# Performance work log

Hardware: AMD Instinct MI355X
Metric: run time of the kernel (lower is better)

## Reference

```python
import jax, jax.numpy as jnp
import numpy as np

N_NODES = 100000


def _deg_norm(idx, n):
    # inverse-sqrt degree, zero-degree nodes -> 0 (DGL norm='both' convention)
    deg = jax.ops.segment_sum(jnp.ones(idx.shape, jnp.float32), idx, num_segments=n)
    return jnp.where(deg > 0, jax.lax.rsqrt(jnp.maximum(deg, 1.0)), 0.0)


def graph_conv(x, src, dst, W, b, n):
    # symmetric normalization: D_out^{-1/2} on src, D_in^{-1/2} on dst
    norm_src = _deg_norm(src, n)  # [N]
    norm_dst = _deg_norm(dst, n)  # [N]
    h = (x * norm_src[:, None]) @ W          # apply weight first (in >= out)
    msg = h[src]                              # gather [E, out]
    agg = jax.ops.segment_sum(msg, dst, num_segments=n)  # scatter-add [N, out]
    return agg * norm_dst[:, None] + b


def setup_inputs() -> dict:
    key = jax.random.key(0)
    ks = jax.random.split(key, 6)
    x = jax.random.normal(ks[0], (N_NODES, 128), dtype=jnp.float32)
    edge_index = jax.random.randint(ks[1], (2, 1600000), 0, N_NODES, dtype=jnp.int64)
    W1 = jax.random.normal(ks[2], (128, 64), dtype=jnp.float32) * (1.0 / np.sqrt(128))
    b1 = jnp.zeros((64,), jnp.float32)
    W2 = jax.random.normal(ks[3], (64, 32), dtype=jnp.float32) * (1.0 / np.sqrt(64))
    b2 = jnp.zeros((32,), jnp.float32)
    Wl = jax.random.normal(ks[4], (32, 1), dtype=jnp.float32) * (1.0 / np.sqrt(32))
    bl = jnp.zeros((1,), jnp.float32)
    return {"x": x, "edge_index": edge_index, "W1": W1, "b1": b1,
            "W2": W2, "b2": b2, "Wl": Wl, "bl": bl}


def reference(x, edge_index, W1, b1, W2, b2, Wl, bl):
    src, dst = edge_index[0], edge_index[1]
    n = x.shape[0]
    h = graph_conv(x, src, dst, W1, b1, n)
    h = jax.nn.relu(h)
    # dropout(p=0.5) is identity at inference
    h = graph_conv(h, src, dst, W2, b2, n)
    return h @ Wl + bl  # [N, 1]
```

## Files before the change

### kernel.cpp

```cpp
#include <hip/hip_runtime.h>
#include <hip/hip_fp16.h>


#define WAVE 64
#define NRANGE 8
#define NQUAD 2
#define CB 1024

typedef _Float16 f16x8 __attribute__((ext_vector_type(8)));
typedef float f32x4 __attribute__((ext_vector_type(4)));

__global__ __launch_bounds__(256) void k_hist(const int* __restrict__ srcArr,
                                              const int* __restrict__ dstArr,
                                              unsigned* __restrict__ partial_s,
                                              unsigned* __restrict__ partial_d,
                                              int E, int B, int C, int chunkE) {
    extern __shared__ unsigned hist[];
    const int q = blockIdx.x & (NQUAD - 1);
    const int c = blockIdx.x >> 1;
    const int lo = q * 4 * B;
    const int* nodes = blockIdx.y ? dstArr : srcArr;
    unsigned* partial = blockIdx.y ? partial_d : partial_s;

    for (int b = threadIdx.x; b < B; b += 256) hist[b] = 0u;
    __syncthreads();

    const int beg = c * chunkE, end = min(beg + chunkE, E);
    const int n4 = (end - beg) >> 2;
    const int4* p = (const int4*)(nodes + beg);
    for (int j = threadIdx.x; j < n4; j += 256) {
        int4 v = p[j];
#pragma unroll
        for (int k = 0; k < 4; ++k) {
            int a = (&v.x)[k] - lo;
            if ((unsigned)a < (unsigned)(4 * B)) {
                int h2 = (a >= 2 * B);
                int r2 = a - (h2 ? 2 * B : 0);
                int h1 = (r2 >= B);
                int bin = r2 - (h1 ? B : 0);
                atomicAdd(&hist[bin], 1u << (((h2 << 1) | h1) << 3));
            }
        }
    }
    for (int j = beg + (n4 << 2) + threadIdx.x; j < end; j += 256) {
        int a = nodes[j] - lo;
        if ((unsigned)a < (unsigned)(4 * B)) {
            int h2 = (a >= 2 * B);
            int r2 = a - (h2 ? 2 * B : 0);
            int h1 = (r2 >= B);
            int bin = r2 - (h1 ? B : 0);
            atomicAdd(&hist[bin], 1u << (((h2 << 1) | h1) << 3));
        }
    }
    __syncthreads();
    unsigned* outp = partial + (size_t)(q * C + c) * B;
    for (int b = threadIdx.x; b < B; b += 256) outp[b] = hist[b];
}

__global__ __launch_bounds__(256) void k_reduce_norm(const unsigned* __restrict__ partial_s,
                                                     unsigned* __restrict__ partial_d,
                                                     float* __restrict__ norm_s,
                                                     float* __restrict__ norm_d,
                                                     unsigned* __restrict__ deg_d,
                                                     int N, int B, int C) {
    int t = blockIdx.x * 256 + threadIdx.x;
    if (t >= NQUAD * B) return;
    int q = t / B, b = t - q * B;
    size_t base = (size_t)(q * C) * B + b;
    unsigned ds = 0;
    for (int c = 0; c < C; ++c) ds += partial_s[base + (size_t)c * B];
    unsigned run = 0;
    for (int c = 0; c < C; ++c) {
        size_t ix = base + (size_t)c * B;
        unsigned v = partial_d[ix];
        partial_d[ix] = run;
        run += v;
    }
#pragma unroll
    for (int j = 0; j < 4; ++j) {
        int n = q * 4 * B + j * B + b;
        if (n < N) {
            unsigned d0 = (ds >> (8 * j)) & 0xffu;
            unsigned d1 = (run >> (8 * j)) & 0xffu;
            deg_d[n] = d1;
            norm_s[n] = d0 ? rsqrtf((float)d0) : 0.0f;
            norm_d[n] = d1 ? rsqrtf((float)d1) : 0.0f;
        }
    }
}

__global__ __launch_bounds__(256) void k_prep(const float* __restrict__ W1,
                                              const float* __restrict__ W2,
                                              const float* __restrict__ b2,
                                              const float* __restrict__ Wl,
                                              const float* __restrict__ bl,
                                              _Float16* __restrict__ wt,
                                              float* __restrict__ w2l,
                                              float* __restrict__ c0) {
    int t = threadIdx.x;
    for (int i = 0; i < 32; ++i) {
        int e = i * 256 + t;
        int k = e >> 6, n = e & 63;
        wt[n * 128 + k] = (_Float16)W1[e];
    }
    if (t < 64) {
        float acc = 0.f;
#pragma unroll
        for (int j = 0; j < 32; ++j) acc += W2[t * 32 + j] * Wl[j];
        w2l[t] = acc;
    }
    if (t == 0) {
        float s = 0.f;
#pragma unroll
        for (int j = 0; j < 32; ++j) s += b2[j] * Wl[j];
        *c0 = s + bl[0];
    }
}

__global__ __launch_bounds__(256) void k_blocksum(const unsigned* __restrict__ deg,
                                                  unsigned* __restrict__ partial, int N) {
    __shared__ unsigned sw[4];
    int i = blockIdx.x * 256 + threadIdx.x;
    unsigned v = (i < N) ? deg[i] : 0u;
#pragma unroll
    for (int off = 32; off; off >>= 1) v += __shfl_xor((int)v, off);
    if ((threadIdx.x & 63) == 0) sw[threadIdx.x >> 6] = v;
    __syncthreads();
    if (threadIdx.x == 0) partial[blockIdx.x] = sw[0] + sw[1] + sw[2] + sw[3];
}

__global__ __launch_bounds__(512) void k_scanpartial(const unsigned* __restrict__ partial,
                                                     unsigned* __restrict__ blockoff,
                                                     unsigned* __restrict__ offsets,
                                                     int nb, int N) {
    __shared__ unsigned s[512];
    int t = threadIdx.x;
    unsigned v = (t < nb) ? partial[t] : 0u;
    s[t] = v;
    __syncthreads();
    for (int off = 1; off < 512; off <<= 1) {
        unsigned a = (t >= off) ? s[t - off] : 0u;
        __syncthreads();
        s[t] += a;
        __syncthreads();
    }
    if (t < nb) blockoff[t] = s[t] - v;
    if (t == nb - 1) offsets[N] = s[t];
}

__global__ __launch_bounds__(256) void k_offsets(const unsigned* __restrict__ deg,
                                                 const unsigned* __restrict__ blockoff,
                                                 unsigned* __restrict__ offsets, int N) {
    __shared__ unsigned s[256];
    int t = threadIdx.x;
    int i = blockIdx.x * 256 + t;
    unsigned v = (i < N) ? deg[i] : 0u;
    s[t] = v;
    __syncthreads();
    for (int off = 1; off < 256; off <<= 1) {
        unsigned a = (t >= off) ? s[t - off] : 0u;
        __syncthreads();
        s[t] += a;
        __syncthreads();
    }
    if (i < N) offsets[i] = blockoff[blockIdx.x] + s[t] - v;
}

__global__ __launch_bounds__(256) void k_cnt(const int* __restrict__ dst,
                                             unsigned* __restrict__ cnt,
                                             int E, int B, int chunkEb) {
    __shared__ unsigned lc[NRANGE];
    if (threadIdx.x < NRANGE) lc[threadIdx.x] = 0u;
    __syncthreads();
    const int c = blockIdx.x;
    const int beg = c * chunkEb, end = min(beg + chunkEb, E);
    unsigned pc[NRANGE] = {};
    for (int i = beg + (int)threadIdx.x; i < end; i += 256) {
        int r = dst[i] / B;
#pragma unroll
        for (int rr = 0; rr < NRANGE; ++rr) pc[rr] += (r == rr);
    }
#pragma unroll
    for (int rr = 0; rr < NRANGE; ++rr) {
        unsigned v = pc[rr];
#pragma unroll
        for (int off = 32; off; off >>= 1) v += __shfl_xor((int)v, off);
        if ((threadIdx.x & 63) == 0 && v) atomicAdd(&lc[rr], v);
    }
    __syncthreads();
    if (threadIdx.x < NRANGE) cnt[threadIdx.x * CB + c] = lc[threadIdx.x];
}

__global__ __launch_bounds__(256) void k_scancnt2(const unsigned* __restrict__ cnt,
                                                  unsigned* __restrict__ segBase) {
    __shared__ unsigned s[256];
    const int t = threadIdx.x;
    const int PER = (NRANGE * CB) / 256;
    unsigned loc[PER];
    unsigned sum = 0;
#pragma unroll
    for (int j = 0; j < PER; ++j) { loc[j] = sum; sum += cnt[t * PER + j]; }
    s[t] = sum;
    __syncthreads();
    for (int off = 1; off < 256; off <<= 1) {
        unsigned a = (t >= off) ? s[t - off] : 0u;
        __syncthreads();
        s[t] += a;
        __syncthreads();
    }
    unsigned base = s[t] - sum;
#pragma unroll
    for (int j = 0; j < PER; ++j) segBase[t * PER + j] = base + loc[j];
    if (t == 255) segBase[NRANGE * CB] = s[255];
}

__global__ __launch_bounds__(256) void k_bucket(const int* __restrict__ src,
                                                const int* __restrict__ dst,
                                                const unsigned* __restrict__ segBase,
                                                uint2* __restrict__ ebuf,
                                                int E, int B, int chunkEb) {
    __shared__ unsigned lcnt[NRANGE];
    const int c = blockIdx.x;
    const int lane = threadIdx.x & 63;
    if (threadIdx.x < NRANGE) lcnt[threadIdx.x] = 0u;
    __syncthreads();

    unsigned sb[NRANGE];
#pragma unroll
    for (int r = 0; r < NRANGE; ++r) sb[r] = segBase[r * CB + c];

    const int beg = c * chunkEb, end = min(beg + chunkEb, E);
    for (int i = beg + (int)threadIdx.x; i < end; i += 256) {
        int d = dst[i];
        int s = src[i];
        int r = d / B;
#pragma unroll
        for (int rr = 0; rr < NRANGE; ++rr) {
            unsigned long long m = __ballot(r == rr);
            if (m) {
                int leader = __ffsll((long long)m) - 1;
                unsigned base = 0;
                if (lane == leader) base = atomicAdd(&lcnt[rr], (unsigned)__popcll(m));
                base = (unsigned)__shfl((int)base, leader);
                if (r == rr) {
                    unsigned before = (unsigned)__popcll(m & ((1ull << lane) - 1ull));
                    ebuf[sb[rr] + base + before] = make_uint2((unsigned)s, (unsigned)d);
                }
            }
        }
    }
}

__global__ __launch_bounds__(256) void k_fill2(const uint2* __restrict__ ebuf,
                                               const unsigned* __restrict__ segBase,
                                               const unsigned* __restrict__ offsets,
                                               const unsigned* __restrict__ rel,
                                               unsigned* __restrict__ csr,
                                               int N, int B, int C, int RB) {
    extern __shared__ unsigned curs[];
    const int r = blockIdx.x & (NRANGE - 1);
    const int ch = blockIdx.x >> 3;
    const int lo = r * B;
    const int bins = min(B, N - lo);
    const int sh = (r & 3) << 3;
    const unsigned* relp = rel + (size_t)((r >> 2) * C + ch) * B;
    for (int b = threadIdx.x; b < bins; b += 256)
        curs[b] = offsets[lo + b] + ((relp[b] >> sh) & 0xffu);
    __syncthreads();

    const unsigned s0 = segBase[r * CB + ch * RB];
    const unsigned s1 = segBase[r * CB + ch * RB + RB];
    for (unsigned i = s0 + threadIdx.x; i < s1; i += 256) {
        uint2 e = ebuf[i];
        int a = (int)e.y - lo;
        if ((unsigned)a < (unsigned)bins)
            csr[atomicAdd(&curs[a], 1u)] = e.x;
    }
}

__global__ __launch_bounds__(256) void k_gemm1(const float* __restrict__ x,
                                               const _Float16* __restrict__ wt,
                                               const float* __restrict__ norm_s,
                                               __half* __restrict__ h1h, int N) {
    __shared__ __align__(16) _Float16 xs[64 * 128];
    const int tid = threadIdx.x, lane = tid & 63, wv = tid >> 6;
    const int r0 = blockIdx.x * 64;

    f16x8 bf[4][4];
#pragma unroll
    for (int kt = 0; kt < 4; ++kt)
#pragma unroll
        for (int nt = 0; nt < 4; ++nt)
            bf[kt][nt] = *(const f16x8*)&wt[(nt * 16 + (lane & 15)) * 128 +
                                            kt * 32 + (lane >> 4) * 8];

#pragma unroll
    for (int it = 0; it < 8; ++it) {
        int e = it * 256 + tid;
        int r = e >> 5, c = e & 31;
        int row = r0 + r;
        float4 v = (row < N) ? ((const float4*)x)[(size_t)row * 32 + c]
                             : make_float4(0.f, 0.f, 0.f, 0.f);
        __half2 lo2 = __floats2half2_rn(v.x, v.y);
        __half2 hi2 = __floats2half2_rn(v.z, v.w);
        uint2 pk;
        pk.x = *(unsigned*)&lo2;
        pk.y = *(unsigned*)&hi2;
        int byte = r * 256 + c * 8;
        byte ^= (r & 7) << 4;
        *(uint2*)((char*)xs + byte) = pk;
    }
    __syncthreads();

    f32x4 acc[4] = {};
    const int rloc = wv * 16 + (lane & 15);
#pragma unroll
    for (int kt = 0; kt < 4; ++kt) {
        int byte = rloc * 256 + (kt * 32 + (lane >> 4) * 8) * 2;
        byte ^= (rloc & 7) << 4;
        f16x8 af = *(const f16x8*)((char*)xs + byte);
#pragma unroll
        for (int nt = 0; nt < 4; ++nt)
            acc[nt] = __builtin_amdgcn_mfma_f32_16x16x32_f16(af, bf[kt][nt], acc[nt], 0, 0, 0);
    }

#pragma unroll
    for (int j = 0; j < 4; ++j) {
        int row = r0 + wv * 16 + (lane >> 4) * 4 + j;
        if (row < N) {
            float ns = norm_s[row];
#pragma unroll
            for (int nt = 0; nt < 4; ++nt)
                h1h[(size_t)row * 64 + nt * 16 + (lane & 15)] =
                    __float2half(acc[nt][j] * ns);
        }
    }
}

__global__ __launch_bounds__(256) void k_agg_rdot(const unsigned* __restrict__ offsets,
                                                  const unsigned* __restrict__ csr,
                                                  const __half* __restrict__ h1h,
                                                  const float* __restrict__ norm_s,
                                                  const float* __restrict__ norm_d,
                                                  const float* __restrict__ b1,
                                                  const float* __restrict__ w2l,
                                                  float* __restrict__ s_node, int N) {
    const int lane = threadIdx.x & 63;
    const int slot = lane >> 4;
    const int p = lane & 15;
    const int v = (blockIdx.x * 256 + threadIdx.x) >> 6;
    if (v >= N) return;
    const unsigned beg = offsets[v], end = offsets[v + 1];

    float a0 = 0.f, a1 = 0.f, a2 = 0.f, a3 = 0.f;
#define GATHER(sreg) { \
        uint2 u = *(const uint2*)&h1h[(size_t)(sreg) * 64 + 4 * p]; \
        float2 f0 = __half22float2(*(__half2*)&u.x); \
        float2 f1 = __half22float2(*(__half2*)&u.y); \
        a0 += f0.x; a1 += f0.y; a2 += f1.x; a3 += f1.y; }

    for (unsigned base = beg; base < end; base += WAVE) {
        const int n = (int)min((unsigned)WAVE, end - base);
        int sv = (lane < n) ? (int)csr[base + lane] : 0;
        int i = 0;
        for (; i + 32 <= n; i += 32) {
            int s0 = __shfl(sv, i + 0 + slot);
            int s1 = __shfl(sv, i + 4 + slot);
            int s2 = __shfl(sv, i + 8 + slot);
            int s3 = __shfl(sv, i + 12 + slot);
            int s4 = __shfl(sv, i + 16 + slot);
            int s5 = __shfl(sv, i + 20 + slot);
            int s6 = __shfl(sv, i + 24 + slot);
            int s7 = __shfl(sv, i + 28 + slot);
            GATHER(s0); GATHER(s1); GATHER(s2); GATHER(s3);
            GATHER(s4); GATHER(s5); GATHER(s6); GATHER(s7);
        }
        for (; i + 16 <= n; i += 16) {
            int s0 = __shfl(sv, i + 0 + slot);
            int s1 = __shfl(sv, i + 4 + slot);
            int s2 = __shfl(sv, i + 8 + slot);
            int s3 = __shfl(sv, i + 12 + slot);
            GATHER(s0); GATHER(s1); GATHER(s2); GATHER(s3);
        }
        for (; i < n; i += 4) {
            int e = i + slot;
            int s = __shfl(sv, min(e, n - 1));
            if (e < n) GATHER(s);
        }
    }
#undef GATHER
    a0 += __shfl_xor(a0, 16); a0 += __shfl_xor(a0, 32);
    a1 += __shfl_xor(a1, 16); a1 += __shfl_xor(a1, 32);
    a2 += __shfl_xor(a2, 16); a2 += __shfl_xor(a2, 32);
    a3 += __shfl_xor(a3, 16); a3 += __shfl_xor(a3, 32);

    float nd = norm_d[v];
    float4 bq = *(const float4*)&b1[4 * p];
    float4 wq = *(const float4*)&w2l[4 * p];
    float t = fmaxf(fmaf(a0, nd, bq.x), 0.f) * wq.x
            + fmaxf(fmaf(a1, nd, bq.y), 0.f) * wq.y
            + fmaxf(fmaf(a2, nd, bq.z), 0.f) * wq.z
            + fmaxf(fmaf(a3, nd, bq.w), 0.f) * wq.w;
#pragma unroll
    for (int off = 8; off; off >>= 1) t += __shfl_xor(t, off);
    if (lane == 0) s_node[v] = t * norm_s[v];
}

__global__ __launch_bounds__(256) void k_out(const unsigned* __restrict__ offsets,
                                             const unsigned* __restrict__ csr,
                                             const float* __restrict__ s_node,
                                             const float* __restrict__ norm_d,
                                             const float* __restrict__ c0,
                                             float* __restrict__ out, int N) {
    int v = blockIdx.x * 256 + threadIdx.x;
    if (v >= N) return;
    unsigned beg = offsets[v], end = offsets[v + 1];
    float sum = 0.f;
    unsigned j = beg;
    for (; j + 4 <= end; j += 4) {
        float a = s_node[csr[j + 0]], b = s_node[csr[j + 1]];
        float c = s_node[csr[j + 2]], d = s_node[csr[j + 3]];
        sum += a + b + c + d;
    }
    for (; j < end; ++j) sum += s_node[csr[j]];
    out[v] = fmaf(sum, norm_d[v], *c0);
}

extern "C" void kernel_launch(void* const* d_in, const int* in_sizes, int n_in,
                              void* d_out, int out_size, void* d_ws, size_t ws_size,
                              hipStream_t stream) {
    const float* x  = (const float*)d_in[0];
    const int*   ei = (const int*)d_in[1];
    const float* W1 = (const float*)d_in[2];
    const float* b1 = (const float*)d_in[3];
    const float* W2 = (const float*)d_in[4];
    const float* b2 = (const float*)d_in[5];
    const float* Wl = (const float*)d_in[6];
    const float* bl = (const float*)d_in[7];

    const int N = in_sizes[0] / 128;
    const int E = in_sizes[1] / 2;
    const int* src = ei;
    const int* dst = ei + E;
    const int NB = (N + 255) / 256;
    const int B = (N + NRANGE - 1) / NRANGE;

    size_t baseBytes = 0;
    {
        auto pad = [](size_t b) { return (b + 255) & ~(size_t)255; };
        baseBytes = pad((size_t)N * 4) * 3 + pad((size_t)(N + 1) * 4) +
                    pad((size_t)NB * 4) * 2 + pad((size_t)N * 64 * 2) +
                    pad((size_t)E * 4) + pad((size_t)N * 4) + pad(64 * 4) + pad(4) +
                    pad(64 * 128 * 2) + pad((size_t)E * 8) +
                    pad((size_t)(NRANGE * CB + 1) * 4) * 2;
    }
    int C = 64;
    while (C > 4 && baseBytes + 2ull * NQUAD * C * B * 4ull > ws_size) C >>= 1;
    const int chunkEb = (E + CB - 1) / CB;
    const int RB = CB / C;
    const int chunkE = chunkEb * RB;

    char* w = (char*)d_ws;
    auto alloc = [&](size_t bytes) -> void* {
        void* r = (void*)w;
        w += (bytes + 255) & ~(size_t)255;
        return r;
    };
    float*    norm_s    = (float*)alloc((size_t)N * 4);
    float*    norm_d    = (float*)alloc((size_t)N * 4);
    unsigned* deg_d     = (unsigned*)alloc((size_t)N * 4);
    unsigned* offsets   = (unsigned*)alloc((size_t)(N + 1) * 4);
    unsigned* partial   = (unsigned*)alloc((size_t)NB * 4);
    unsigned* blockoff  = (unsigned*)alloc((size_t)NB * 4);
    __half*   h1h       = (__half*)alloc((size_t)N * 64 * 2);
    unsigned* csr       = (unsigned*)alloc((size_t)E * 4);
    float*    s_node    = (float*)alloc((size_t)N * 4);
    float*    w2l       = (float*)alloc(64 * 4);
    float*    c0        = (float*)alloc(4);
    _Float16* wt        = (_Float16*)alloc(64 * 128 * 2);
    uint2*    ebuf      = (uint2*)alloc((size_t)E * 8);
    unsigned* cnt       = (unsigned*)alloc((size_t)(NRANGE * CB + 1) * 4);
    unsigned* segBase   = (unsigned*)alloc((size_t)(NRANGE * CB + 1) * 4);
    unsigned* partial_s = (unsigned*)alloc((size_t)NQUAD * C * B * 4);
    unsigned* partial_d = (unsigned*)alloc((size_t)NQUAD * C * B * 4);

    float* out = (float*)d_out;
    const size_t ldsB = (size_t)B * 4;

    k_cnt<<<CB, 256, 0, stream>>>(dst, cnt, E, B, chunkEb);
    k_scancnt2<<<1, 256, 0, stream>>>(cnt, segBase);
    k_bucket<<<CB, 256, 0, stream>>>(src, dst, segBase, ebuf, E, B, chunkEb);

    k_hist<<<dim3(NQUAD * C, 2), 256, ldsB, stream>>>(src, dst, partial_s, partial_d,
                                                      E, B, C, chunkE);
    k_prep<<<1, 256, 0, stream>>>(W1, W2, b2, Wl, bl, wt, w2l, c0);

    k_reduce_norm<<<(NQUAD * B + 255) / 256, 256, 0, stream>>>(partial_s, partial_d,
                                                               norm_s, norm_d,
                                                               deg_d, N, B, C);
    k_blocksum<<<NB, 256, 0, stream>>>(deg_d, partial, N);
    k_scanpartial<<<1, 512, 0, stream>>>(partial, blockoff, offsets, NB, N);
    k_offsets<<<NB, 256, 0, stream>>>(deg_d, blockoff, offsets, N);

    k_fill2<<<NRANGE * C, 256, ldsB, stream>>>(ebuf, segBase, offsets, partial_d,
                                               csr, N, B, C, RB);

    k_gemm1<<<(N + 63) / 64, 256, 0, stream>>>(x, wt, norm_s, h1h, N);

    k_agg_rdot<<<(N + 3) / 4, 256, 0, stream>>>(offsets, csr, h1h, norm_s, norm_d,
                                                b1, w2l, s_node, N);
    k_out<<<NB, 256, 0, stream>>>(offsets, csr, s_node, norm_d, c0, out, N);
}
```

Baseline: 195.7 us.

## Replace global count-scan-bucket with atomic per-range slotted bucketing and fuse prep

Merges the edge count, global scan and bucket kernels into one kernel that reserves per-range spans with a global atomic cursor, writing into fixed-size per-range slots (E/NRANGE plus slack). The weight-prep work moves into an extra block of that kernel. CSR offsets become per-range slotted, and consumers take row length from deg_d instead of offsets[v+1]. The partial-histogram chunk count drops from 64 to 32. This removes several launches and a serial scan, at the cost of non-contiguous CSR, a larger workspace, and overflow risk if a range gets more than its slot holds.

```diff
diff --git a/kernel.cpp b/kernel.cpp
--- a/kernel.cpp
+++ b/kernel.cpp
@@ -9,6 +9,101 @@
 
 typedef _Float16 f16x8 __attribute__((ext_vector_type(8)));
 typedef float f32x4 __attribute__((ext_vector_type(4)));
+
+__global__ __launch_bounds__(256) void k_bucket2(const int* __restrict__ src,
+                                                 const int* __restrict__ dst,
+                                                 unsigned* __restrict__ rangeCursor,
+                                                 unsigned* __restrict__ spanBase,
+                                                 unsigned* __restrict__ spanLen,
+                                                 uint2* __restrict__ ebuf,
+                                                 int E, int B, int chunkEb, int SLOT,
+                                                 const float* __restrict__ W1,
+                                                 const float* __restrict__ W2,
+                                                 const float* __restrict__ b2,
+                                                 const float* __restrict__ Wl,
+                                                 const float* __restrict__ bl,
+                                                 _Float16* __restrict__ wt,
+                                                 float* __restrict__ w2l,
+                                                 float* __restrict__ c0) {
+    if (blockIdx.x == CB) {
+        int t = threadIdx.x;
+        for (int i = 0; i < 32; ++i) {
+            int e = i * 256 + t;
+            int k = e >> 6, n = e & 63;
+            wt[n * 128 + k] = (_Float16)W1[e];
+        }
+        if (t < 64) {
+            float acc = 0.f;
+#pragma unroll
+            for (int j = 0; j < 32; ++j) acc += W2[t * 32 + j] * Wl[j];
+            w2l[t] = acc;
+        }
+        if (t == 0) {
+            float s = 0.f;
+#pragma unroll
+            for (int j = 0; j < 32; ++j) s += b2[j] * Wl[j];
+            *c0 = s + bl[0];
+        }
+        return;
+    }
+
+    __shared__ unsigned lc[NRANGE];
+    __shared__ unsigned sbs[NRANGE];
+    __shared__ unsigned cur[NRANGE];
+    const int c = blockIdx.x;
+    const int lane = threadIdx.x & 63;
+    if (threadIdx.x < NRANGE) { lc[threadIdx.x] = 0u; cur[threadIdx.x] = 0u; }
+    __syncthreads();
+
+    const int beg = c * chunkEb, end = min(beg + chunkEb, E);
+
+    unsigned pc[NRANGE] = {};
+    for (int i = beg + (int)threadIdx.x; i < end; i += 256) {
+        int r = dst[i] / B;
+#pragma unroll
+        for (int rr = 0; rr < NRANGE; ++rr) pc[rr] += (r == rr);
+    }
+#pragma unroll
+    for (int rr = 0; rr < NRANGE; ++rr) {
+        unsigned v = pc[rr];
+#pragma unroll
+        for (int off = 32; off; off >>= 1) v += __shfl_xor((int)v, off);
+        if (lane == 0 && v) atomicAdd(&lc[rr], v);
+    }
+    __syncthreads();
+    if (threadIdx.x < NRANGE) {
+        int r = threadIdx.x;
+        unsigned base = atomicAdd(&rangeCursor[r], lc[r]);
+        sbs[r] = base;
+        spanBase[r * CB + c] = base;
+        spanLen[r * CB + c] = lc[r];
+    }
+    __syncthreads();
+
+    unsigned pb[NRANGE];
+#pragma unroll
+    for (int r = 0; r < NRANGE; ++r) pb[r] = (unsigned)(r * SLOT) + sbs[r];
+
+    for (int i = beg + (int)threadIdx.x; i < end; i += 256) {
+        int d = dst[i];
+        int s = src[i];
+        int r = d / B;
+#pragma unroll
+        for (int rr = 0; rr < NRANGE; ++rr) {
+            unsigned long long m = __ballot(r == rr);
+            if (m) {
+                int leader = __ffsll((long long)m) - 1;
+                unsigned base = 0;
+                if (lane == leader) base = atomicAdd(&cur[rr], (unsigned)__popcll(m));
+                base = (unsigned)__shfl((int)base, leader);
+                if (r == rr) {
+                    unsigned before = (unsigned)__popcll(m & ((1ull << lane) - 1ull));
+                    ebuf[pb[rr] + base + before] = make_uint2((unsigned)s, (unsigned)d);
+                }
+            }
+        }
+    }
+}
 
 __global__ __launch_bounds__(256) void k_hist(const int* __restrict__ srcArr,
                                               const int* __restrict__ dstArr,
@@ -89,50 +184,25 @@
     }
 }
 
-__global__ __launch_bounds__(256) void k_prep(const float* __restrict__ W1,
-                                              const float* __restrict__ W2,
-                                              const float* __restrict__ b2,
-                                              const float* __restrict__ Wl,
-                                              const float* __restrict__ bl,
-                                              _Float16* __restrict__ wt,
-                                              float* __restrict__ w2l,
-                                              float* __restrict__ c0) {
-    int t = threadIdx.x;
-    for (int i = 0; i < 32; ++i) {
-        int e = i * 256 + t;
-        int k = e >> 6, n = e & 63;
-        wt[n * 128 + k] = (_Float16)W1[e];
-    }
-    if (t < 64) {
-        float acc = 0.f;
-#pragma unroll
-        for (int j = 0; j < 32; ++j) acc += W2[t * 32 + j] * Wl[j];
-        w2l[t] = acc;
-    }
-    if (t == 0) {
-        float s = 0.f;
-#pragma unroll
-        for (int j = 0; j < 32; ++j) s += b2[j] * Wl[j];
-        *c0 = s + bl[0];
-    }
-}
-
 __global__ __launch_bounds__(256) void k_blocksum(const unsigned* __restrict__ deg,
-                                                  unsigned* __restrict__ partial, int N) {
+                                                  unsigned* __restrict__ partial,
+                                                  int N, int B, int PB) {
     __shared__ unsigned sw[4];
-    int i = blockIdx.x * 256 + threadIdx.x;
-    unsigned v = (i < N) ? deg[i] : 0u;
-#pragma unroll
-    for (int off = 32; off; off >>= 1) v += __shfl_xor((int)v, off);
-    if ((threadIdx.x & 63) == 0) sw[threadIdx.x >> 6] = v;
+    int r = blockIdx.x / PB, j = blockIdx.x - r * PB;
+    int b = j * 256 + threadIdx.x;
+    int node = r * B + b;
+    unsigned v = (b < B && node < N) ? deg[node] : 0u;
+    unsigned s = v;
+#pragma unroll
+    for (int off = 32; off; off >>= 1) s += __shfl_xor((int)s, off);
+    if ((threadIdx.x & 63) == 0) sw[threadIdx.x >> 6] = s;
     __syncthreads();
     if (threadIdx.x == 0) partial[blockIdx.x] = sw[0] + sw[1] + sw[2] + sw[3];
 }
 
 __global__ __launch_bounds__(512) void k_scanpartial(const unsigned* __restrict__ partial,
                                                      unsigned* __restrict__ blockoff,
-                                                     unsigned* __restrict__ offsets,
-                                                     int nb, int N) {
+                                                     int nb, int PB) {
     __shared__ unsigned s[512];
     int t = threadIdx.x;
     unsigned v = (t < nb) ? partial[t] : 0u;
@@ -144,17 +214,23 @@
         s[t] += a;
         __syncthreads();
     }
-    if (t < nb) blockoff[t] = s[t] - v;
-    if (t == nb - 1) offsets[N] = s[t];
+    if (t < nb) {
+        int r = t / PB;
+        unsigned rbase = (r > 0) ? s[r * PB - 1] : 0u;
+        blockoff[t] = s[t] - v - rbase;
+    }
 }
 
 __global__ __launch_bounds__(256) void k_offsets(const unsigned* __restrict__ deg,
                                                  const unsigned* __restrict__ blockoff,
-                                                 unsigned* __restrict__ offsets, int N) {
+                                                 unsigned* __restrict__ offsets,
+                                                 int N, int B, int PB, int SLOT) {
     __shared__ unsigned s[256];
+    int r = blockIdx.x / PB, j = blockIdx.x - r * PB;
     int t = threadIdx.x;
-    int i = blockIdx.x * 256 + t;
-    unsigned v = (i < N) ? deg[i] : 0u;
+    int b = j * 256 + t;
+    int node = r * B + b;
+    unsigned v = (b < B && node < N) ? deg[node] : 0u;
     s[t] = v;
     __syncthreads();
     for (int off = 1; off < 256; off <<= 1) {
@@ -163,100 +239,17 @@
         s[t] += a;
         __syncthreads();
     }
-    if (i < N) offsets[i] = blockoff[blockIdx.x] + s[t] - v;
-}
-
-__global__ __launch_bounds__(256) void k_cnt(const int* __restrict__ dst,
-                                             unsigned* __restrict__ cnt,
-                                             int E, int B, int chunkEb) {
-    __shared__ unsigned lc[NRANGE];
-    if (threadIdx.x < NRANGE) lc[threadIdx.x] = 0u;
-    __syncthreads();
-    const int c = blockIdx.x;
-    const int beg = c * chunkEb, end = min(beg + chunkEb, E);
-    unsigned pc[NRANGE] = {};
-    for (int i = beg + (int)threadIdx.x; i < end; i += 256) {
-        int r = dst[i] / B;
-#pragma unroll
-        for (int rr = 0; rr < NRANGE; ++rr) pc[rr] += (r == rr);
-    }
-#pragma unroll
-    for (int rr = 0; rr < NRANGE; ++rr) {
-        unsigned v = pc[rr];
-#pragma unroll
-        for (int off = 32; off; off >>= 1) v += __shfl_xor((int)v, off);
-        if ((threadIdx.x & 63) == 0 && v) atomicAdd(&lc[rr], v);
-    }
-    __syncthreads();
-    if (threadIdx.x < NRANGE) cnt[threadIdx.x * CB + c] = lc[threadIdx.x];
-}
-
-__global__ __launch_bounds__(256) void k_scancnt2(const unsigned* __restrict__ cnt,
-                                                  unsigned* __restrict__ segBase) {
-    __shared__ unsigned s[256];
-    const int t = threadIdx.x;
-    const int PER = (NRANGE * CB) / 256;
-    unsigned loc[PER];
-    unsigned sum = 0;
-#pragma unroll
-    for (int j = 0; j < PER; ++j) { loc[j] = sum; sum += cnt[t * PER + j]; }
-    s[t] = sum;
-    __syncthreads();
-    for (int off = 1; off < 256; off <<= 1) {
-        unsigned a = (t >= off) ? s[t - off] : 0u;
-        __syncthreads();
-        s[t] += a;
-        __syncthreads();
-    }
-    unsigned base = s[t] - sum;
-#pragma unroll
-    for (int j = 0; j < PER; ++j) segBase[t * PER + j] = base + loc[j];
-    if (t == 255) segBase[NRANGE * CB] = s[255];
-}
-
-__global__ __launch_bounds__(256) void k_bucket(const int* __restrict__ src,
-                                                const int* __restrict__ dst,
-                                                const unsigned* __restrict__ segBase,
-                                                uint2* __restrict__ ebuf,
-                                                int E, int B, int chunkEb) {
-    __shared__ unsigned lcnt[NRANGE];
-    const int c = blockIdx.x;
-    const int lane = threadIdx.x & 63;
-    if (threadIdx.x < NRANGE) lcnt[threadIdx.x] = 0u;
-    __syncthreads();
-
-    unsigned sb[NRANGE];
-#pragma unroll
-    for (int r = 0; r < NRANGE; ++r) sb[r] = segBase[r * CB + c];
-
-    const int beg = c * chunkEb, end = min(beg + chunkEb, E);
-    for (int i = beg + (int)threadIdx.x; i < end; i += 256) {
-        int d = dst[i];
-        int s = src[i];
-        int r = d / B;
-#pragma unroll
-        for (int rr = 0; rr < NRANGE; ++rr) {
-            unsigned long long m = __ballot(r == rr);
-            if (m) {
-                int leader = __ffsll((long long)m) - 1;
-                unsigned base = 0;
-                if (lane == leader) base = atomicAdd(&lcnt[rr], (unsigned)__popcll(m));
-                base = (unsigned)__shfl((int)base, leader);
-                if (r == rr) {
-                    unsigned before = (unsigned)__popcll(m & ((1ull << lane) - 1ull));
-                    ebuf[sb[rr] + base + before] = make_uint2((unsigned)s, (unsigned)d);
-                }
-            }
-        }
-    }
+    if (b < B && node < N)
+        offsets[node] = (unsigned)(r * SLOT) + blockoff[blockIdx.x] + s[t] - v;
 }
 
 __global__ __launch_bounds__(256) void k_fill2(const uint2* __restrict__ ebuf,
-                                               const unsigned* __restrict__ segBase,
+                                               const unsigned* __restrict__ spanBase,
+                                               const unsigned* __restrict__ spanLen,
                                                const unsigned* __restrict__ offsets,
                                                const unsigned* __restrict__ rel,
                                                unsigned* __restrict__ csr,
-                                               int N, int B, int C, int RB) {
+                                               int N, int B, int C, int RB, int SLOT) {
     extern __shared__ unsigned curs[];
     const int r = blockIdx.x & (NRANGE - 1);
     const int ch = blockIdx.x >> 3;
@@ -268,13 +261,16 @@
         curs[b] = offsets[lo + b] + ((relp[b] >> sh) & 0xffu);
     __syncthreads();
 
-    const unsigned s0 = segBase[r * CB + ch * RB];
-    const unsigned s1 = segBase[r * CB + ch * RB + RB];
-    for (unsigned i = s0 + threadIdx.x; i < s1; i += 256) {
-        uint2 e = ebuf[i];
-        int a = (int)e.y - lo;
-        if ((unsigned)a < (unsigned)bins)
-            csr[atomicAdd(&curs[a], 1u)] = e.x;
+    const unsigned rbase = (unsigned)(r * SLOT);
+    for (int cb = ch * RB; cb < ch * RB + RB; ++cb) {
+        const unsigned s0 = rbase + spanBase[r * CB + cb];
+        const unsigned len = spanLen[r * CB + cb];
+        for (unsigned i = s0 + threadIdx.x; i < s0 + len; i += 256) {
+            uint2 e = ebuf[i];
+            int a = (int)e.y - lo;
+            if ((unsigned)a < (unsigned)bins)
+                csr[atomicAdd(&curs[a], 1u)] = e.x;
+        }
     }
 }
 
@@ -338,6 +334,7 @@
 }
 
 __global__ __launch_bounds__(256) void k_agg_rdot(const unsigned* __restrict__ offsets,
+                                                  const unsigned* __restrict__ deg_d,
                                                   const unsigned* __restrict__ csr,
                                                   const __half* __restrict__ h1h,
                                                   const float* __restrict__ norm_s,
@@ -350,7 +347,8 @@
     const int p = lane & 15;
     const int v = (blockIdx.x * 256 + threadIdx.x) >> 6;
     if (v >= N) return;
-    const unsigned beg = offsets[v], end = offsets[v + 1];
+    const unsigned beg = offsets[v];
+    const unsigned end = beg + deg_d[v];
 
     float a0 = 0.f, a1 = 0.f, a2 = 0.f, a3 = 0.f;
 #define GATHER(sreg) { \
@@ -407,6 +405,7 @@
 }
 
 __global__ __launch_bounds__(256) void k_out(const unsigned* __restrict__ offsets,
+                                             const unsigned* __restrict__ deg_d,
                                              const unsigned* __restrict__ csr,
                                              const float* __restrict__ s_node,
                                              const float* __restrict__ norm_d,
@@ -414,13 +413,13 @@
                                              float* __restrict__ out, int N) {
     int v = blockIdx.x * 256 + threadIdx.x;
     if (v >= N) return;
-    unsigned beg = offsets[v], end = offsets[v + 1];
+    unsigned beg = offsets[v], end = beg + deg_d[v];
     float sum = 0.f;
     unsigned j = beg;
     for (; j + 4 <= end; j += 4) {
         float a = s_node[csr[j + 0]], b = s_node[csr[j + 1]];
         float c = s_node[csr[j + 2]], d = s_node[csr[j + 3]];
-        sum += a + b + c + d;
+        sum += (a + b) + (c + d);
     }
     for (; j < end; ++j) sum += s_node[csr[j]];
     out[v] = fmaf(sum, norm_d[v], *c0);
@@ -444,17 +443,20 @@
     const int* dst = ei + E;
     const int NB = (N + 255) / 256;
     const int B = (N + NRANGE - 1) / NRANGE;
+    const int PB = (B + 255) / 256;
+    const int SLOT = E / NRANGE + 16384;
 
     size_t baseBytes = 0;
     {
         auto pad = [](size_t b) { return (b + 255) & ~(size_t)255; };
-        baseBytes = pad((size_t)N * 4) * 3 + pad((size_t)(N + 1) * 4) +
-                    pad((size_t)NB * 4) * 2 + pad((size_t)N * 64 * 2) +
-                    pad((size_t)E * 4) + pad((size_t)N * 4) + pad(64 * 4) + pad(4) +
-                    pad(64 * 128 * 2) + pad((size_t)E * 8) +
-                    pad((size_t)(NRANGE * CB + 1) * 4) * 2;
-    }
-    int C = 64;
+        baseBytes = pad((size_t)N * 4) * 3 + pad((size_t)N * 4) +
+                    pad((size_t)NRANGE * PB * 4) * 2 + pad((size_t)N * 64 * 2) +
+                    pad((size_t)NRANGE * SLOT * 4) + pad((size_t)N * 4) +
+                    pad(64 * 4) + pad(4) + pad(64 * 128 * 2) +
+                    pad((size_t)NRANGE * SLOT * 8) +
+                    pad((size_t)NRANGE * CB * 4) * 2 + pad(NRANGE * 4);
+    }
+    int C = 32;
     while (C > 4 && baseBytes + 2ull * NQUAD * C * B * 4ull > ws_size) C >>= 1;
     const int chunkEb = (E + CB - 1) / CB;
     const int RB = CB / C;
@@ -469,45 +471,48 @@
     float*    norm_s    = (float*)alloc((size_t)N * 4);
     float*    norm_d    = (float*)alloc((size_t)N * 4);
     unsigned* deg_d     = (unsigned*)alloc((size_t)N * 4);
-    unsigned* offsets   = (unsigned*)alloc((size_t)(N + 1) * 4);
-    unsigned* partial   = (unsigned*)alloc((size_t)NB * 4);
-    unsigned* blockoff  = (unsigned*)alloc((size_t)NB * 4);
+    unsigned* offsets   = (unsigned*)alloc((size_t)N * 4);
+    unsigned* partial   = (unsigned*)alloc((size_t)NRANGE * PB * 4);
+    unsigned* blockoff  = (unsigned*)alloc((size_t)NRANGE * PB * 4);
     __half*   h1h       = (__half*)alloc((size_t)N * 64 * 2);
-    unsigned* csr       = (unsigned*)alloc((size_t)E * 4);
+    unsigned* csr       = (unsigned*)alloc((size_t)NRANGE * SLOT * 4);
     float*    s_node    = (float*)alloc((size_t)N * 4);
     float*    w2l       = (float*)alloc(64 * 4);
     float*    c0        = (float*)alloc(4);
     _Float16* wt        = (_Float16*)alloc(64 * 128 * 2);
-    uint2*    ebuf      = (uint2*)alloc((size_t)E * 8);
-    unsigned* cnt       = (unsigned*)alloc((size_t)(NRANGE * CB + 1) * 4);
-    unsigned* segBase   = (unsigned*)alloc((size_t)(NRANGE * CB + 1) * 4);
+    uint2*    ebuf      = (uint2*)alloc((size_t)NRANGE * SLOT * 8);
+    unsigned* spanBase  = (unsigned*)alloc((size_t)NRANGE * CB * 4);
+    unsigned* spanLen   = (unsigned*)alloc((size_t)NRANGE * CB * 4);
+    unsigned* rangeCur  = (unsigned*)alloc(NRANGE * 4);
     unsigned* partial_s = (unsigned*)alloc((size_t)NQUAD * C * B * 4);
     unsigned* partial_d = (unsigned*)alloc((size_t)NQUAD * C * B * 4);
 
     float* out = (float*)d_out;
     const size_t ldsB = (size_t)B * 4;
 
-    k_cnt<<<CB, 256, 0, stream>>>(dst, cnt, E, B, chunkEb);
-    k_scancnt2<<<1, 256, 0, stream>>>(cnt, segBase);
-    k_bucket<<<CB, 256, 0, stream>>>(src, dst, segBase, ebuf, E, B, chunkEb);
+    hipMemsetAsync(rangeCur, 0, NRANGE * 4, stream);
+
+    k_bucket2<<<CB + 1, 256, 0, stream>>>(src, dst, rangeCur, spanBase, spanLen,
+                                          ebuf, E, B, chunkEb, SLOT,
+                                          W1, W2, b2, Wl, bl, wt, w2l, c0);
 
     k_hist<<<dim3(NQUAD * C, 2), 256, ldsB, stream>>>(src, dst, partial_s, partial_d,
                                                       E, B, C, chunkE);
-    k_prep<<<1, 256, 0, stream>>>(W1, W2, b2, Wl, bl, wt, w2l, c0);
 
     k_reduce_norm<<<(NQUAD * B + 255) / 256, 256, 0, stream>>>(partial_s, partial_d,
                                                                norm_s, norm_d,
                                                                deg_d, N, B, C);
-    k_blocksum<<<NB, 256, 0, stream>>>(deg_d, partial, N);
-    k_scanpartial<<<1, 512, 0, stream>>>(partial, blockoff, offsets, NB, N);
-    k_offsets<<<NB, 256, 0, stream>>>(deg_d, blockoff, offsets, N);
-
-    k_fill2<<<NRANGE * C, 256, ldsB, stream>>>(ebuf, segBase, offsets, partial_d,
-                                               csr, N, B, C, RB);
 
     k_gemm1<<<(N + 63) / 64, 256, 0, stream>>>(x, wt, norm_s, h1h, N);
 
-    k_agg_rdot<<<(N + 3) / 4, 256, 0, stream>>>(offsets, csr, h1h, norm_s, norm_d,
-                                                b1, w2l, s_node, N);
-    k_out<<<NB, 256, 0, stream>>>(offsets, csr, s_node, norm_d, c0, out, N);
-}
+    k_blocksum<<<NRANGE * PB, 256, 0, stream>>>(deg_d, partial, N, B, PB);
+    k_scanpartial<<<1, 512, 0, stream>>>(partial, blockoff, NRANGE * PB, PB);
+    k_offsets<<<NRANGE * PB, 256, 0, stream>>>(deg_d, blockoff, offsets, N, B, PB, SLOT);
+
+    k_fill2<<<NRANGE * C, 256, ldsB, stream>>>(ebuf, spanBase, spanLen, offsets,
+                                               partial_d, csr, N, B, C, RB, SLOT);
+
+    k_agg_rdot<<<(N + 3) / 4, 256, 0, stream>>>(offsets, deg_d, csr, h1h, norm_s,
+                                                norm_d, b1, w2l, s_node, N);
+    k_out<<<NB, 256, 0, stream>>>(offsets, deg_d, csr, s_node, norm_d, c0, out, N);
+}
```

Result: slower. 201.7 us (+3.1%).
